# Kernel tuning notes

Measured on AMD Instinct MI355X. Metric: run time of the kernel, lower is better.

## Reference

```python
import jax, jax.numpy as jnp
import numpy as np

N_NODES = 50000
IN_DIM = 128
OUT_DIM = 128
HEADS = 4
HEAD_DIM = OUT_DIM // HEADS
N_EDGES = 800000
LN_EPS = 1e-5
NEG_SLOPE = 0.2


def setup_inputs() -> dict:
    key = jax.random.key(0)
    ks = jax.random.split(key, 8)
    x = jax.random.normal(ks[0], (N_NODES, IN_DIM), dtype=jnp.float32)
    edge_index = jax.random.randint(ks[1], (2, N_EDGES), 0, N_NODES, dtype=jnp.int64)
    s = 1.0 / np.sqrt(IN_DIM)
    W = jax.random.uniform(ks[2], (IN_DIM, HEADS * HEAD_DIM), jnp.float32, -s, s)
    att_src = jax.random.uniform(ks[3], (HEADS, HEAD_DIM), jnp.float32, -s, s)
    att_dst = jax.random.uniform(ks[4], (HEADS, HEAD_DIM), jnp.float32, -s, s)
    bias = jnp.zeros((OUT_DIM,), jnp.float32)
    gamma = jnp.ones((OUT_DIM,), jnp.float32)
    beta = jnp.zeros((OUT_DIM,), jnp.float32)
    return {"x": x, "edge_index": edge_index, "W": W, "att_src": att_src,
            "att_dst": att_dst, "bias": bias, "gamma": gamma, "beta": beta}


def reference(x, edge_index, W, att_src, att_dst, bias, gamma, beta):
    N = x.shape[0]
    H, C = att_src.shape
    # add self-loops (PyG GATConv default)
    loops = jnp.arange(N, dtype=edge_index.dtype)
    src = jnp.concatenate([edge_index[0], loops])  # [E+N]
    dst = jnp.concatenate([edge_index[1], loops])

    h = (x @ W).reshape(N, H, C)                      # [N,H,C]
    a_src = jnp.einsum('nhc,hc->nh', h, att_src)      # [N,H]
    a_dst = jnp.einsum('nhc,hc->nh', h, att_dst)

    e = jax.nn.leaky_relu(a_src[src] + a_dst[dst], NEG_SLOPE)   # [E+N,H]
    emax = jax.ops.segment_max(e, dst, num_segments=N)          # [N,H]
    ex = jnp.exp(e - emax[dst])
    denom = jax.ops.segment_sum(ex, dst, num_segments=N)
    alpha = ex / denom[dst]                                     # [E+N,H]

    msg = h[src] * alpha[:, :, None]                            # [E+N,H,C]
    out = jax.ops.segment_sum(msg, dst, num_segments=N).reshape(N, H * C) + bias

    # LayerNorm
    mu = out.mean(-1, keepdims=True)
    var = ((out - mu) ** 2).mean(-1, keepdims=True)
    hn = (out - mu) / jnp.sqrt(var + LN_EPS) * gamma + beta

    # residual is Identity (in_dim == out_dim); GELU exact; dropout = eval identity
    return jax.nn.gelu(hn + x, approximate=False)
```

## Files before the change

### kernel.cpp

```cpp
#include <hip/hip_runtime.h>
#include <math.h>

#define N_NODES 50000
#define HEADS 4
#define NEG_SLOPE 0.2f
#define LN_EPS 1e-5f
#define SLOTS 80
#define GR 64
#define EPB 2048
#define DSH 8
#define NB 196
#define CAP 40
#define HBW 40

typedef short short8 __attribute__((ext_vector_type(8)));
typedef float f32x4 __attribute__((ext_vector_type(4)));


__device__ __forceinline__ short f2bf(float f) {
    unsigned u = __float_as_uint(f);
    return (short)((u + 0x7fffu + ((u >> 16) & 1u)) >> 16);
}

__device__ __forceinline__ int detect_is64(const int* __restrict__ ei, int t, int* s_flag) {
    if (t < 64) {
        int nz = (ei[2 * t + 1] != 0) ? 1 : 0;
        unsigned long long b = __ballot(nz);
        if (t == 0) *s_flag = (b == 0ULL) ? 1 : 0;
    }
    __syncthreads();
    return *s_flag;
}

__device__ __forceinline__ float s8f(unsigned u, int p) {
    return (float)((int)(u << (24 - 8 * p)) >> 24);
}

__device__ __forceinline__ float edge_w(float v) {
    v = v > 0.f ? v : NEG_SLOPE * v;
    return __expf(v);
}


__global__ __launch_bounds__(256, 4) void gemm_scatter_kernel(
    const float* __restrict__ x, const float* __restrict__ W,
    const float* __restrict__ att_src, const float* __restrict__ att_dst,
    unsigned* __restrict__ hb, float* __restrict__ a_dst,
    const int* __restrict__ ei, int E, int nScatter, int nGemm,
    unsigned* __restrict__ staging, int* __restrict__ scnt) {
    __shared__ __align__(16) char smem[40960];
    const int t = threadIdx.x;
    const int b = (int)blockIdx.x;

    const bool isBin = (b % 3) == 0;
    const int rid = isBin ? (b / 3) : (2 * (b / 3) + (b % 3) - 1);

    if (isBin) {
        if (rid >= nScatter) return;
        int is64 = detect_is64(ei, t, (int*)smem);
        int* lcnt = (int*)smem + 64;
        for (int i = t; i < NB; i += 256) lcnt[i] = 0;
        __syncthreads();

        const int e0 = rid * EPB + t * 8;
        int ss[8], dd[8];
        if (e0 + 8 <= E) {
            if (is64) {
                const uint4* ps4 = (const uint4*)(ei + 2 * (size_t)e0);
                const uint4* pd4 = (const uint4*)(ei + 2 * ((size_t)E + e0));
#pragma unroll
                for (int u = 0; u < 4; ++u) {
                    uint4 qs = ps4[u], qd = pd4[u];
                    ss[2 * u] = (int)qs.x; ss[2 * u + 1] = (int)qs.z;
                    dd[2 * u] = (int)qd.x; dd[2 * u + 1] = (int)qd.z;
                }
            } else {
                const uint4* ps4 = (const uint4*)(ei + e0);
                const uint4* pd4 = (const uint4*)(ei + (size_t)E + e0);
#pragma unroll
                for (int u = 0; u < 2; ++u) {
                    uint4 qs = ps4[u], qd = pd4[u];
                    ss[4 * u] = (int)qs.x; ss[4 * u + 1] = (int)qs.y;
                    ss[4 * u + 2] = (int)qs.z; ss[4 * u + 3] = (int)qs.w;
                    dd[4 * u] = (int)qd.x; dd[4 * u + 1] = (int)qd.y;
                    dd[4 * u + 2] = (int)qd.z; dd[4 * u + 3] = (int)qd.w;
                }
            }
        } else {
#pragma unroll
            for (int u = 0; u < 8; ++u) {
                int e = e0 + u;
                if (e < E) {
                    if (is64) { ss[u] = ei[2 * e]; dd[u] = ei[2 * (E + e)]; }
                    else      { ss[u] = ei[e];     dd[u] = ei[E + e]; }
                } else { ss[u] = -1; dd[u] = 0; }
            }
        }
#pragma unroll
        for (int u = 0; u < 8; ++u) {
            if (ss[u] < 0) continue;
            int bkt = dd[u] >> DSH;
            int p = atomicAdd(&lcnt[bkt], 1);
            if (p < CAP)
                staging[((size_t)bkt * nScatter + rid) * CAP + p] =
                    (unsigned)ss[u] | ((unsigned)dd[u] << 16);
        }
        __syncthreads();
        for (int i = t; i < NB; i += 256)
            scnt[(size_t)i * nScatter + rid] = min(lcnt[i], CAP);
        return;
    }

    if (rid >= nGemm) return;
    const int rowBase = rid * GR;
    const int l = t & 63;
    const int wv = t >> 6;

    {
        const int nlo = l & 7, khi = l >> 3;
        for (int i = 0; i < 8; ++i) {
            int tile = wv + 4 * i;
            int n = (tile & 15) * 8 + nlo;
            int k8 = (tile >> 4) * 8 + khi;
            short8 pk;
#pragma unroll
            for (int jj = 0; jj < 8; ++jj)
                pk[jj] = f2bf(W[(k8 * 8 + jj) * 128 + n]);
            int us = (k8 & 8) | ((k8 & 7) ^ (n & 7));
            *(short8*)(smem + n * 256 + us * 16) = pk;
        }
    }
    __syncthreads();

    const int g = l >> 4;
    const int c = l & 15;

    f32x4 acc[8];
#pragma unroll
    for (int ct = 0; ct < 8; ++ct) acc[ct] = {0.f, 0.f, 0.f, 0.f};

    {
        int arow = rowBase + wv * 16 + c;
        if (arow >= N_NODES) arow = N_NODES - 1;
        const float* xrow = x + (size_t)arow * 128;
#pragma unroll
        for (int kk = 0; kk < 4; ++kk) {
            float4 xa = *(const float4*)(xrow + kk * 32 + g * 8);
            float4 xb = *(const float4*)(xrow + kk * 32 + g * 8 + 4);
            short8 af;
            af[0] = f2bf(xa.x); af[1] = f2bf(xa.y); af[2] = f2bf(xa.z); af[3] = f2bf(xa.w);
            af[4] = f2bf(xb.x); af[5] = f2bf(xb.y); af[6] = f2bf(xb.z); af[7] = f2bf(xb.w);
#pragma unroll
            for (int ct = 0; ct < 8; ++ct) {
                int n = ct * 16 + c;
                int u = kk * 4 + g;
                int us = (u & 8) | ((u & 7) ^ (n & 7));
                short8 bf = *(const short8*)(smem + n * 256 + us * 16);
                acc[ct] = __builtin_amdgcn_mfma_f32_16x16x32_bf16(af, bf, acc[ct], 0, 0, 0);
            }
        }
    }

    char* ep = smem + 32768 + wv * 2048;
    float asA[4], asB[4], adA[4], adB[4];
#pragma unroll
    for (int h = 0; h < 4; ++h) {
        asA[h] = att_src[h * 32 + c];
        asB[h] = att_src[h * 32 + 16 + c];
        adA[h] = att_dst[h * 32 + c];
        adB[h] = att_dst[h * 32 + 16 + c];
    }
#pragma unroll
    for (int r = 0; r < 4; ++r) {
        float v[8];
#pragma unroll
        for (int ct = 0; ct < 8; ++ct) v[ct] = acc[ct][r];

        float m = fabsf(v[0]);
#pragma unroll
        for (int ct = 1; ct < 8; ++ct) m = fmaxf(m, fabsf(v[ct]));
#pragma unroll
        for (int o = 1; o < 16; o <<= 1) m = fmaxf(m, __shfl_xor(m, o, 64));
        m = fmaxf(m, 1e-20f);
        const float inv = 127.0f / m;

        float sp[4], dp[4];
#pragma unroll
        for (int h = 0; h < 4; ++h) {
            sp[h] = v[2 * h] * asA[h] + v[2 * h + 1] * asB[h];
            dp[h] = v[2 * h] * adA[h] + v[2 * h + 1] * adB[h];
        }
#pragma unroll
        for (int o = 1; o < 16; o <<= 1) {
#pragma unroll
            for (int h = 0; h < 4; ++h) {
                sp[h] += __shfl_xor(sp[h], o, 64);
                dp[h] += __shfl_xor(dp[h], o, 64);
            }
        }
        const int row_l = g * 4 + r;
        const int row = rowBase + wv * 16 + row_l;
        if (c == 0 && row < N_NODES) {
            const float hs = m * (1.0f / 127.0f);
            float4* rw = (float4*)(hb + (size_t)row * HBW + 32);
            rw[0] = make_float4(sp[0], hs, sp[1], hs);
            rw[1] = make_float4(sp[2], hs, sp[3], hs);
            a_dst[row * 4 + 0] = dp[0]; a_dst[row * 4 + 1] = dp[1];
            a_dst[row * 4 + 2] = dp[2]; a_dst[row * 4 + 3] = dp[3];
        }
#pragma unroll
        for (int ct = 0; ct < 8; ++ct) {
            int q = __float2int_rn(v[ct] * inv);
            ep[row_l * 128 + ct * 16 + c] = (char)q;
        }
    }

#pragma unroll
    for (int w8 = 0; w8 < 8; ++w8) {
        int idx = w8 * 64 + l;
        int row_l = idx >> 5, tx = idx & 31;
        unsigned word = *(const unsigned*)(ep + row_l * 128 + tx * 4);
        int row = rowBase + wv * 16 + row_l;
        if (row < N_NODES) hb[(size_t)row * HBW + tx] = word;
    }
}

__global__ __launch_bounds__(256) void build_kernel(
    const unsigned* __restrict__ staging, const int* __restrict__ scnt,
    int nScatter, int* __restrict__ cnt, unsigned short* __restrict__ esrc) {
    __shared__ int lcnt2[256];
    const int B = blockIdx.x;
    const int t = threadIdx.x;
    lcnt2[t] = 0;
    __syncthreads();

    for (int blk = t; blk < nScatter; blk += 256) {
        const int c = scnt[(size_t)B * nScatter + blk];
        const unsigned* cell = staging + ((size_t)B * nScatter + blk) * CAP;
        for (int j = 0; j < c; j += 4) {
            uint4 q = *(const uint4*)(cell + j);
            const int m = c - j;
            {
                int d = (int)(q.x >> 16);
                int p = atomicAdd(&lcnt2[d & 255], 1);
                if (p < SLOTS) esrc[(size_t)d * SLOTS + p] = (unsigned short)(q.x & 0xffffu);
            }
            if (m > 1) {
                int d = (int)(q.y >> 16);
                int p = atomicAdd(&lcnt2[d & 255], 1);
                if (p < SLOTS) esrc[(size_t)d * SLOTS + p] = (unsigned short)(q.y & 0xffffu);
            }
            if (m > 2) {
                int d = (int)(q.z >> 16);
                int p = atomicAdd(&lcnt2[d & 255], 1);
                if (p < SLOTS) esrc[(size_t)d * SLOTS + p] = (unsigned short)(q.z & 0xffffu);
            }
            if (m > 3) {
                int d = (int)(q.w >> 16);
                int p = atomicAdd(&lcnt2[d & 255], 1);
                if (p < SLOTS) esrc[(size_t)d * SLOTS + p] = (unsigned short)(q.w & 0xffffu);
            }
        }
    }
    __syncthreads();
    const int d = (B << DSH) + t;
    if (d < N_NODES) cnt[d] = lcnt2[t];
}

__global__ __launch_bounds__(256) void gat_fused_kernel(
    const int* __restrict__ cnt, const unsigned short* __restrict__ esrc,
    const float* __restrict__ a_dst,
    const unsigned* __restrict__ hb,
    const float* __restrict__ bias, const float* __restrict__ x,
    const float* __restrict__ gamma, const float* __restrict__ beta,
    float* __restrict__ out) {
    const int t = threadIdx.x;
    const int l = t & 63;
    const int wv = t >> 6;
    const int g = l >> 4;
    const int j = l & 15;
    const int n = blockIdx.x * 16 + wv * 4 + g;
    const int hh = j >> 2;

    const uint2* hb2 = (const uint2*)hb;

    const float adst_me = a_dst[(n << 2) + hh];
    uint2 rS = hb2[(unsigned)(n * 20 + 16 + hh)];
    float ps = edge_w(__uint_as_float(rS.x) + adst_me);

    uint2 hvS = hb2[(unsigned)(n * 20 + j)];
    {
        const float uS = ps * __uint_as_float(rS.y);
        float acc0 = uS * s8f(hvS.x, 0), acc1 = uS * s8f(hvS.x, 1);
        float acc2 = uS * s8f(hvS.x, 2), acc3 = uS * s8f(hvS.x, 3);
        float acc4 = uS * s8f(hvS.y, 0), acc5 = uS * s8f(hvS.y, 1);
        float acc6 = uS * s8f(hvS.y, 2), acc7 = uS * s8f(hvS.y, 3);

        const int deg = min(cnt[n], SLOTS);
        const unsigned short* row = esrc + n * SLOTS;

        for (int base = 0; base < deg; base += 8) {
            const int rem = deg - base;
            uint4 q = *(const uint4*)(row + base);
            int s0 = (int)(q.x & 0xffffu);
            int s1 = (rem > 1) ? (int)(q.x >> 16) : n;
            int s2 = (rem > 2) ? (int)(q.y & 0xffffu) : n;
            int s3 = (rem > 3) ? (int)(q.y >> 16) : n;
            int s4 = (rem > 4) ? (int)(q.z & 0xffffu) : n;
            int s5 = (rem > 5) ? (int)(q.z >> 16) : n;
            int s6 = (rem > 6) ? (int)(q.w & 0xffffu) : n;
            int s7 = (rem > 7) ? (int)(q.w >> 16) : n;

            uint2 r0 = hb2[(unsigned)(s0 * 20 + 16 + hh)];
            uint2 r1 = hb2[(unsigned)(s1 * 20 + 16 + hh)];
            uint2 r2 = hb2[(unsigned)(s2 * 20 + 16 + hh)];
            uint2 r3 = hb2[(unsigned)(s3 * 20 + 16 + hh)];
            uint2 r4 = hb2[(unsigned)(s4 * 20 + 16 + hh)];
            uint2 r5 = hb2[(unsigned)(s5 * 20 + 16 + hh)];
            uint2 r6 = hb2[(unsigned)(s6 * 20 + 16 + hh)];
            uint2 r7 = hb2[(unsigned)(s7 * 20 + 16 + hh)];
            uint2 h0 = hb2[(unsigned)(s0 * 20 + j)];
            uint2 h1 = hb2[(unsigned)(s1 * 20 + j)];
            uint2 h2 = hb2[(unsigned)(s2 * 20 + j)];
            uint2 h3 = hb2[(unsigned)(s3 * 20 + j)];
            uint2 h4 = hb2[(unsigned)(s4 * 20 + j)];
            uint2 h5 = hb2[(unsigned)(s5 * 20 + j)];
            uint2 h6 = hb2[(unsigned)(s6 * 20 + j)];
            uint2 h7 = hb2[(unsigned)(s7 * 20 + j)];

            float w0 = edge_w(__uint_as_float(r0.x) + adst_me);
            float w1 = (rem > 1) ? edge_w(__uint_as_float(r1.x) + adst_me) : 0.f;
            float w2 = (rem > 2) ? edge_w(__uint_as_float(r2.x) + adst_me) : 0.f;
            float w3 = (rem > 3) ? edge_w(__uint_as_float(r3.x) + adst_me) : 0.f;
            float w4 = (rem > 4) ? edge_w(__uint_as_float(r4.x) + adst_me) : 0.f;
            float w5 = (rem > 5) ? edge_w(__uint_as_float(r5.x) + adst_me) : 0.f;
            float w6 = (rem > 6) ? edge_w(__uint_as_float(r6.x) + adst_me) : 0.f;
            float w7 = (rem > 7) ? edge_w(__uint_as_float(r7.x) + adst_me) : 0.f;
            ps += (w0 + w1 + w2 + w3) + (w4 + w5 + w6 + w7);

            float u0 = w0 * __uint_as_float(r0.y), u1 = w1 * __uint_as_float(r1.y);
            float u2 = w2 * __uint_as_float(r2.y), u3 = w3 * __uint_as_float(r3.y);
            float u4 = w4 * __uint_as_float(r4.y), u5 = w5 * __uint_as_float(r5.y);
            float u6 = w6 * __uint_as_float(r6.y), u7 = w7 * __uint_as_float(r7.y);

            acc0 += u0 * s8f(h0.x, 0) + u1 * s8f(h1.x, 0) + u2 * s8f(h2.x, 0) + u3 * s8f(h3.x, 0)
                  + u4 * s8f(h4.x, 0) + u5 * s8f(h5.x, 0) + u6 * s8f(h6.x, 0) + u7 * s8f(h7.x, 0);
            acc1 += u0 * s8f(h0.x, 1) + u1 * s8f(h1.x, 1) + u2 * s8f(h2.x, 1) + u3 * s8f(h3.x, 1)
                  + u4 * s8f(h4.x, 1) + u5 * s8f(h5.x, 1) + u6 * s8f(h6.x, 1) + u7 * s8f(h7.x, 1);
            acc2 += u0 * s8f(h0.x, 2) + u1 * s8f(h1.x, 2) + u2 * s8f(h2.x, 2) + u3 * s8f(h3.x, 2)
                  + u4 * s8f(h4.x, 2) + u5 * s8f(h5.x, 2) + u6 * s8f(h6.x, 2) + u7 * s8f(h7.x, 2);
            acc3 += u0 * s8f(h0.x, 3) + u1 * s8f(h1.x, 3) + u2 * s8f(h2.x, 3) + u3 * s8f(h3.x, 3)
                  + u4 * s8f(h4.x, 3) + u5 * s8f(h5.x, 3) + u6 * s8f(h6.x, 3) + u7 * s8f(h7.x, 3);
            acc4 += u0 * s8f(h0.y, 0) + u1 * s8f(h1.y, 0) + u2 * s8f(h2.y, 0) + u3 * s8f(h3.y, 0)
                  + u4 * s8f(h4.y, 0) + u5 * s8f(h5.y, 0) + u6 * s8f(h6.y, 0) + u7 * s8f(h7.y, 0);
            acc5 += u0 * s8f(h0.y, 1) + u1 * s8f(h1.y, 1) + u2 * s8f(h2.y, 1) + u3 * s8f(h3.y, 1)
                  + u4 * s8f(h4.y, 1) + u5 * s8f(h5.y, 1) + u6 * s8f(h6.y, 1) + u7 * s8f(h7.y, 1);
            acc6 += u0 * s8f(h0.y, 2) + u1 * s8f(h1.y, 2) + u2 * s8f(h2.y, 2) + u3 * s8f(h3.y, 2)
                  + u4 * s8f(h4.y, 2) + u5 * s8f(h5.y, 2) + u6 * s8f(h6.y, 2) + u7 * s8f(h7.y, 2);
            acc7 += u0 * s8f(h0.y, 3) + u1 * s8f(h1.y, 3) + u2 * s8f(h2.y, 3) + u3 * s8f(h3.y, 3)
                  + u4 * s8f(h4.y, 3) + u5 * s8f(h5.y, 3) + u6 * s8f(h6.y, 3) + u7 * s8f(h7.y, 3);
        }

        const float inv = 1.0f / ps;
        const float4* bias4 = (const float4*)bias;
        float4 bA = bias4[j * 2], bB = bias4[j * 2 + 1];
        float v0 = acc0 * inv + bA.x, v1 = acc1 * inv + bA.y;
        float v2 = acc2 * inv + bA.z, v3 = acc3 * inv + bA.w;
        float v4 = acc4 * inv + bB.x, v5 = acc5 * inv + bB.y;
        float v6 = acc6 * inv + bB.z, v7 = acc7 * inv + bB.w;

        float s1 = v0 + v1 + v2 + v3 + v4 + v5 + v6 + v7;
        float s2 = v0 * v0 + v1 * v1 + v2 * v2 + v3 * v3 +
                   v4 * v4 + v5 * v5 + v6 * v6 + v7 * v7;
#pragma unroll
        for (int o = 1; o < 16; o <<= 1) {
            s1 += __shfl_xor(s1, o, 64);
            s2 += __shfl_xor(s2, o, 64);
        }
        float mu = s1 * (1.0f / 128.0f);
        float var = s2 * (1.0f / 128.0f) - mu * mu;
        float rstd = rsqrtf(var + LN_EPS);

        const float4* gamma4 = (const float4*)gamma;
        const float4* beta4 = (const float4*)beta;
        const float4* x4 = (const float4*)x;
        float4 gA = gamma4[j * 2], gB = gamma4[j * 2 + 1];
        float4 eA = beta4[j * 2], eB = beta4[j * 2 + 1];
        float4 xA = x4[(size_t)n * 32 + j * 2], xB = x4[(size_t)n * 32 + j * 2 + 1];

        float r0f = (v0 - mu) * rstd * gA.x + eA.x + xA.x;
        float r1f = (v1 - mu) * rstd * gA.y + eA.y + xA.y;
        float r2f = (v2 - mu) * rstd * gA.z + eA.z + xA.z;
        float r3f = (v3 - mu) * rstd * gA.w + eA.w + xA.w;
        float r4f = (v4 - mu) * rstd * gB.x + eB.x + xB.x;
        float r5f = (v5 - mu) * rstd * gB.y + eB.y + xB.y;
        float r6f = (v6 - mu) * rstd * gB.z + eB.z + xB.z;
        float r7f = (v7 - mu) * rstd * gB.w + eB.w + xB.w;

        const float k = 0.70710678118654752440f;
        float4 oA = make_float4(0.5f * r0f * (1.0f + erff(r0f * k)),
                                0.5f * r1f * (1.0f + erff(r1f * k)),
                                0.5f * r2f * (1.0f + erff(r2f * k)),
                                0.5f * r3f * (1.0f + erff(r3f * k)));
        float4 oB = make_float4(0.5f * r4f * (1.0f + erff(r4f * k)),
                                0.5f * r5f * (1.0f + erff(r5f * k)),
                                0.5f * r6f * (1.0f + erff(r6f * k)),
                                0.5f * r7f * (1.0f + erff(r7f * k)));
        float4* out4 = (float4*)out;
        out4[(size_t)n * 32 + j * 2] = oA;
        out4[(size_t)n * 32 + j * 2 + 1] = oB;
    }
}


extern "C" void kernel_launch(void* const* d_in, const int* in_sizes, int n_in,
                              void* d_out, int out_size, void* d_ws, size_t ws_size,
                              hipStream_t stream) {
    const float* x       = (const float*)d_in[0];
    const int*   ei      = (const int*)d_in[1];
    const float* W       = (const float*)d_in[2];
    const float* att_src = (const float*)d_in[3];
    const float* att_dst = (const float*)d_in[4];
    const float* bias    = (const float*)d_in[5];
    const float* gamma   = (const float*)d_in[6];
    const float* beta    = (const float*)d_in[7];
    float* out = (float*)d_out;
    const int E = in_sizes[1] / 2;

    unsigned* hb         = (unsigned*)d_ws;
    float* a_dst         = (float*)(hb + (size_t)N_NODES * HBW);
    int*   cnt           = (int*)(a_dst + N_NODES * 4);
    unsigned short* esrc = (unsigned short*)(cnt + N_NODES);

    const int nScatter = (E + EPB - 1) / EPB;
    unsigned* staging    = (unsigned*)(esrc + (size_t)N_NODES * SLOTS);
    int* scnt            = (int*)(staging + (size_t)NB * nScatter * CAP);

    const int nGemm = (N_NODES + GR - 1) / GR;
    int total = 3 * nScatter;
    const int needGemm = 3 * ((nGemm + 1) / 2);
    if (needGemm > total) total = needGemm;

    gemm_scatter_kernel<<<total, 256, 0, stream>>>(
        x, W, att_src, att_dst, hb, a_dst, ei, E, nScatter, nGemm,
        staging, scnt);
    build_kernel<<<NB, 256, 0, stream>>>(staging, scnt, nScatter, cnt, esrc);
    gat_fused_kernel<<<N_NODES / 16, 256, 0, stream>>>(cnt, esrc, a_dst, hb,
                                                       bias, x, gamma, beta, out);
}
```

Before: 150.9 us.

## Stage scatter cells in LDS and split node records from int8 features

The scatter blocks now bin edges into a shared-memory cell array and copy it to a block-major staging layout with contiguous vector stores, replacing scattered global writes. The build kernel reads with the transposed indexing to match. Separately, the per-node hidden buffer is split into a 128-byte int8 feature row plus a separate 32-byte attention/scale record, so gathered rows are aligned to cache lines. The cost is that the build kernel's reads become strided across blocks, and each gathered edge now touches two separate arrays.

```diff
diff --git a/kernel.cpp b/kernel.cpp
--- a/kernel.cpp
+++ b/kernel.cpp
@@ -11,7 +11,6 @@
 #define DSH 8
 #define NB 196
 #define CAP 40
-#define HBW 40
 
 typedef short short8 __attribute__((ext_vector_type(8)));
 typedef float f32x4 __attribute__((ext_vector_type(4)));
@@ -45,7 +44,7 @@
 __global__ __launch_bounds__(256, 4) void gemm_scatter_kernel(
     const float* __restrict__ x, const float* __restrict__ W,
     const float* __restrict__ att_src, const float* __restrict__ att_dst,
-    unsigned* __restrict__ hb, float* __restrict__ a_dst,
+    unsigned* __restrict__ hb, float* __restrict__ rec, float* __restrict__ a_dst,
     const int* __restrict__ ei, int E, int nScatter, int nGemm,
     unsigned* __restrict__ staging, int* __restrict__ scnt) {
     __shared__ __align__(16) char smem[40960];
@@ -59,6 +58,7 @@
         if (rid >= nScatter) return;
         int is64 = detect_is64(ei, t, (int*)smem);
         int* lcnt = (int*)smem + 64;
+        unsigned* cells = (unsigned*)(smem + 1056);
         for (int i = t; i < NB; i += 256) lcnt[i] = 0;
         __syncthreads();
 
@@ -102,12 +102,14 @@
             int bkt = dd[u] >> DSH;
             int p = atomicAdd(&lcnt[bkt], 1);
             if (p < CAP)
-                staging[((size_t)bkt * nScatter + rid) * CAP + p] =
-                    (unsigned)ss[u] | ((unsigned)dd[u] << 16);
+                cells[bkt * CAP + p] = (unsigned)ss[u] | ((unsigned)dd[u] << 16);
         }
         __syncthreads();
+        uint4* dst4 = (uint4*)(staging + (size_t)rid * NB * CAP);
+        const uint4* src4 = (const uint4*)cells;
+        for (int i = t; i < NB * CAP / 4; i += 256) dst4[i] = src4[i];
         for (int i = t; i < NB; i += 256)
-            scnt[(size_t)i * nScatter + rid] = min(lcnt[i], CAP);
+            scnt[(size_t)rid * NB + i] = min(lcnt[i], CAP);
         return;
     }
 
@@ -202,7 +204,7 @@
         const int row = rowBase + wv * 16 + row_l;
         if (c == 0 && row < N_NODES) {
             const float hs = m * (1.0f / 127.0f);
-            float4* rw = (float4*)(hb + (size_t)row * HBW + 32);
+            float4* rw = (float4*)(rec + (size_t)row * 8);
             rw[0] = make_float4(sp[0], hs, sp[1], hs);
             rw[1] = make_float4(sp[2], hs, sp[3], hs);
             a_dst[row * 4 + 0] = dp[0]; a_dst[row * 4 + 1] = dp[1];
@@ -221,7 +223,7 @@
         int row_l = idx >> 5, tx = idx & 31;
         unsigned word = *(const unsigned*)(ep + row_l * 128 + tx * 4);
         int row = rowBase + wv * 16 + row_l;
-        if (row < N_NODES) hb[(size_t)row * HBW + tx] = word;
+        if (row < N_NODES) hb[(size_t)row * 32 + tx] = word;
     }
 }
 
@@ -235,8 +237,8 @@
     __syncthreads();
 
     for (int blk = t; blk < nScatter; blk += 256) {
-        const int c = scnt[(size_t)B * nScatter + blk];
-        const unsigned* cell = staging + ((size_t)B * nScatter + blk) * CAP;
+        const int c = scnt[(size_t)blk * NB + B];
+        const unsigned* cell = staging + ((size_t)blk * NB + B) * CAP;
         for (int j = 0; j < c; j += 4) {
             uint4 q = *(const uint4*)(cell + j);
             const int m = c - j;
@@ -269,7 +271,7 @@
 
 __global__ __launch_bounds__(256) void gat_fused_kernel(
     const int* __restrict__ cnt, const unsigned short* __restrict__ esrc,
-    const float* __restrict__ a_dst,
+    const float* __restrict__ rec, const float* __restrict__ a_dst,
     const unsigned* __restrict__ hb,
     const float* __restrict__ bias, const float* __restrict__ x,
     const float* __restrict__ gamma, const float* __restrict__ beta,
@@ -283,12 +285,13 @@
     const int hh = j >> 2;
 
     const uint2* hb2 = (const uint2*)hb;
+    const uint2* rec2 = (const uint2*)rec;
 
     const float adst_me = a_dst[(n << 2) + hh];
-    uint2 rS = hb2[(unsigned)(n * 20 + 16 + hh)];
+    uint2 rS = rec2[(unsigned)(n * 4 + hh)];
     float ps = edge_w(__uint_as_float(rS.x) + adst_me);
 
-    uint2 hvS = hb2[(unsigned)(n * 20 + j)];
+    uint2 hvS = hb2[(unsigned)(n * 16 + j)];
     {
         const float uS = ps * __uint_as_float(rS.y);
         float acc0 = uS * s8f(hvS.x, 0), acc1 = uS * s8f(hvS.x, 1);
@@ -311,22 +314,22 @@
             int s6 = (rem > 6) ? (int)(q.w & 0xffffu) : n;
             int s7 = (rem > 7) ? (int)(q.w >> 16) : n;
 
-            uint2 r0 = hb2[(unsigned)(s0 * 20 + 16 + hh)];
-            uint2 r1 = hb2[(unsigned)(s1 * 20 + 16 + hh)];
-            uint2 r2 = hb2[(unsigned)(s2 * 20 + 16 + hh)];
-            uint2 r3 = hb2[(unsigned)(s3 * 20 + 16 + hh)];
-            uint2 r4 = hb2[(unsigned)(s4 * 20 + 16 + hh)];
-            uint2 r5 = hb2[(unsigned)(s5 * 20 + 16 + hh)];
-            uint2 r6 = hb2[(unsigned)(s6 * 20 + 16 + hh)];
-            uint2 r7 = hb2[(unsigned)(s7 * 20 + 16 + hh)];
-            uint2 h0 = hb2[(unsigned)(s0 * 20 + j)];
-            uint2 h1 = hb2[(unsigned)(s1 * 20 + j)];
-            uint2 h2 = hb2[(unsigned)(s2 * 20 + j)];
-            uint2 h3 = hb2[(unsigned)(s3 * 20 + j)];
-            uint2 h4 = hb2[(unsigned)(s4 * 20 + j)];
-            uint2 h5 = hb2[(unsigned)(s5 * 20 + j)];
-            uint2 h6 = hb2[(unsigned)(s6 * 20 + j)];
-            uint2 h7 = hb2[(unsigned)(s7 * 20 + j)];
+            uint2 r0 = rec2[(unsigned)(s0 * 4 + hh)];
+            uint2 r1 = rec2[(unsigned)(s1 * 4 + hh)];
+            uint2 r2 = rec2[(unsigned)(s2 * 4 + hh)];
+            uint2 r3 = rec2[(unsigned)(s3 * 4 + hh)];
+            uint2 r4 = rec2[(unsigned)(s4 * 4 + hh)];
+            uint2 r5 = rec2[(unsigned)(s5 * 4 + hh)];
+            uint2 r6 = rec2[(unsigned)(s6 * 4 + hh)];
+            uint2 r7 = rec2[(unsigned)(s7 * 4 + hh)];
+            uint2 h0 = hb2[(unsigned)(s0 * 16 + j)];
+            uint2 h1 = hb2[(unsigned)(s1 * 16 + j)];
+            uint2 h2 = hb2[(unsigned)(s2 * 16 + j)];
+            uint2 h3 = hb2[(unsigned)(s3 * 16 + j)];
+            uint2 h4 = hb2[(unsigned)(s4 * 16 + j)];
+            uint2 h5 = hb2[(unsigned)(s5 * 16 + j)];
+            uint2 h6 = hb2[(unsigned)(s6 * 16 + j)];
+            uint2 h7 = hb2[(unsigned)(s7 * 16 + j)];
 
             float w0 = edge_w(__uint_as_float(r0.x) + adst_me);
             float w1 = (rem > 1) ? edge_w(__uint_as_float(r1.x) + adst_me) : 0.f;
@@ -428,13 +431,14 @@
     const int E = in_sizes[1] / 2;
 
     unsigned* hb         = (unsigned*)d_ws;
-    float* a_dst         = (float*)(hb + (size_t)N_NODES * HBW);
+    float* rec           = (float*)(hb + (size_t)N_NODES * 32);
+    float* a_dst         = rec + (size_t)N_NODES * 8;
     int*   cnt           = (int*)(a_dst + N_NODES * 4);
     unsigned short* esrc = (unsigned short*)(cnt + N_NODES);
 
     const int nScatter = (E + EPB - 1) / EPB;
     unsigned* staging    = (unsigned*)(esrc + (size_t)N_NODES * SLOTS);
-    int* scnt            = (int*)(staging + (size_t)NB * nScatter * CAP);
+    int* scnt            = (int*)(staging + (size_t)nScatter * NB * CAP);
 
     const int nGemm = (N_NODES + GR - 1) / GR;
     int total = 3 * nScatter;
@@ -442,9 +446,9 @@
     if (needGemm > total) total = needGemm;
 
     gemm_scatter_kernel<<<total, 256, 0, stream>>>(
-        x, W, att_src, att_dst, hb, a_dst, ei, E, nScatter, nGemm,
+        x, W, att_src, att_dst, hb, rec, a_dst, ei, E, nScatter, nGemm,
         staging, scnt);
     build_kernel<<<NB, 256, 0, stream>>>(staging, scnt, nScatter, cnt, esrc);
-    gat_fused_kernel<<<N_NODES / 16, 256, 0, stream>>>(cnt, esrc, a_dst, hb,
+    gat_fused_kernel<<<N_NODES / 16, 256, 0, stream>>>(cnt, esrc, rec, a_dst, hb,
                                                        bias, x, gamma, beta, out);
 }
```

Result: faster. 145.5 us (-3.5%).
